# Optimization experiments

Hardware: AMD Instinct MI355X
Metric: run time of the kernel (lower is better)

The kernel has to match this reference:

```python
import jax, jax.numpy as jnp
import numpy as np

RES = 16; NC = 256; NCP = 1024; KNN = 32; SIGMA = 0.1
DM = 256; NH = 8; FF = 1024; NLAYERS = 2
E = NC * 8 * (RES // 8) ** 2
EH = 8
B = 4; N = 65536


def setup_inputs() -> dict:
    key = jax.random.key(0)
    ks = jax.random.split(key, 16)
    s = 0.02
    def w(k, shape):
        return jax.random.normal(k, shape, jnp.float32) * s
    inp = {}
    inp['pc'] = jax.random.normal(ks[0], (B, N, 3), jnp.float32)
    inp['pe_w1'] = w(ks[1], (3, 128)); inp['pe_b1'] = jnp.zeros((128,), jnp.float32)
    inp['pe_w2'] = w(ks[2], (128, 128)); inp['pe_b2'] = jnp.zeros((128,), jnp.float32)
    inp['t_qkv_w'] = w(ks[3], (NLAYERS, DM, 3 * DM)); inp['t_qkv_b'] = jnp.zeros((NLAYERS, 3 * DM), jnp.float32)
    inp['t_out_w'] = w(ks[4], (NLAYERS, DM, DM)); inp['t_out_b'] = jnp.zeros((NLAYERS, DM), jnp.float32)
    inp['t_ln1_s'] = jnp.ones((NLAYERS, DM), jnp.float32); inp['t_ln1_b'] = jnp.zeros((NLAYERS, DM), jnp.float32)
    inp['t_ff1_w'] = w(ks[5], (NLAYERS, DM, FF)); inp['t_ff1_b'] = jnp.zeros((NLAYERS, FF), jnp.float32)
    inp['t_ff2_w'] = w(ks[6], (NLAYERS, FF, DM)); inp['t_ff2_b'] = jnp.zeros((NLAYERS, DM), jnp.float32)
    inp['t_ln2_s'] = jnp.ones((NLAYERS, DM), jnp.float32); inp['t_ln2_b'] = jnp.zeros((NLAYERS, DM), jnp.float32)
    inp['c1_w'] = w(ks[7], (2 * NC, NC, 3, 3)); inp['c1_b'] = jnp.zeros((2 * NC,), jnp.float32)
    inp['c2_w'] = w(ks[8], (4 * NC, 2 * NC, 3, 3)); inp['c2_b'] = jnp.zeros((4 * NC,), jnp.float32)
    inp['c3_w'] = w(ks[9], (8 * NC, 4 * NC, 3, 3)); inp['c3_b'] = jnp.zeros((8 * NC,), jnp.float32)
    inp['x_qkv_w'] = w(ks[10], (E, 3 * E)); inp['x_qkv_b'] = jnp.zeros((3 * E,), jnp.float32)
    inp['x_out_w'] = w(ks[11], (E, E)); inp['x_out_b'] = jnp.zeros((E,), jnp.float32)
    return inp


def _layernorm(x, s, b):
    m = x.mean(-1, keepdims=True)
    v = ((x - m) ** 2).mean(-1, keepdims=True)
    return (x - m) / jnp.sqrt(v + 1e-5) * s + b


def _mha(x, qkv_w, qkv_b, out_w, out_b, nh):
    Bq, S, D = x.shape
    dh = D // nh
    qkv = x @ qkv_w + qkv_b
    q, k, v = jnp.split(qkv, 3, axis=-1)
    def sp(t):
        return t.reshape(Bq, S, nh, dh).transpose(0, 2, 1, 3)
    q, k, v = sp(q), sp(k), sp(v)
    a = jax.nn.softmax(jnp.einsum('bhqd,bhkd->bhqk', q, k) / jnp.sqrt(jnp.float32(dh)), axis=-1)
    o = jnp.einsum('bhqk,bhkd->bhqd', a, v).transpose(0, 2, 1, 3).reshape(Bq, S, D)
    return o @ out_w + out_b


def _density(pc):
    # faithful to source: distance to the FIRST k points (unsorted), not kNN
    d = jnp.linalg.norm(pc[:, :, None, :] - pc[:, None, :KNN, :], axis=-1)  # (B,N,k)
    return jnp.exp(-2.0 * SIGMA ** 2 / (d * d + 1e-6)).mean(axis=-1)


def _fps_indices(pc, density):
    # incremental min-dist FPS: selects identical points to the original O(N*K^2) loop
    def one(pc_b, dens_b):
        first = jnp.argmax(dens_b)
        mind = jnp.linalg.norm(pc_b - pc_b[first], axis=-1)
        def step(mind, _):
            idx = jnp.argmax(mind)
            d = jnp.linalg.norm(pc_b - pc_b[idx], axis=-1)
            return jnp.minimum(mind, d), idx
        _, rest = jax.lax.scan(step, mind, None, length=NCP - 1)
        return jnp.concatenate([first[None], rest])
    return jax.vmap(one)(pc, density)


def _forward(pc, idx, pe_w1, pe_b1, pe_w2, pe_b2, t_qkv_w, t_qkv_b, t_out_w, t_out_b,
             t_ln1_s, t_ln1_b, t_ff1_w, t_ff1_b, t_ff2_w, t_ff2_b, t_ln2_s, t_ln2_b,
             c1_w, c1_b, c2_w, c2_b, c3_w, c3_b, x_qkv_w, x_qkv_b, x_out_w, x_out_b):
    Bq = pc.shape[0]
    centers = jnp.take_along_axis(pc, idx[:, :, None], axis=1)  # (B,K,3)
    # point encoder MLP -> (B,K,128)
    f = jax.nn.relu(centers @ pe_w1 + pe_b1) @ pe_w2 + pe_b2
    # sinusoidal pos-emb per axis, mean over xyz -> (B,K,128)
    half = 64
    freqs = jnp.exp(jnp.arange(half, dtype=jnp.float32) * (-np.log(10000.0) / (half - 1)))
    e = centers[..., None] * freqs  # (B,K,3,64)
    pos = jnp.concatenate([jnp.sin(e), jnp.cos(e)], axis=-1).mean(axis=2)
    x = jnp.concatenate([f, pos], axis=-1)  # (B,K,256)
    # 2-layer post-LN transformer encoder
    for l in range(NLAYERS):
        h = _mha(x, t_qkv_w[l], t_qkv_b[l], t_out_w[l], t_out_b[l], NH)
        x = _layernorm(x + h, t_ln1_s[l], t_ln1_b[l])
        h = jax.nn.relu(x @ t_ff1_w[l] + t_ff1_b[l]) @ t_ff2_w[l] + t_ff2_b[l]
        x = _layernorm(x + h, t_ln2_s[l], t_ln2_b[l])
    # scatter-add features onto three planes
    L = pc.max() - pc.min()
    def grid(c):
        return jnp.clip(((c + L / 2) / L * RES).astype(jnp.int32), 0, RES - 1)
    gx = grid(centers[..., 0]); gy = grid(centers[..., 1]); gz = grid(centers[..., 2])
    tri = jnp.zeros((Bq, 3, RES, RES, DM), jnp.float32)  # channels last for scatter
    bi = jnp.arange(Bq)[:, None]
    tri = tri.at[bi, 0, gy, gx].add(x)
    tri = tri.at[bi, 1, gz, gy].add(x)
    tri = tri.at[bi, 2, gz, gx].add(x)
    tri = tri.transpose(0, 1, 4, 2, 3)  # (B,3,C,R,R)
    z = tri.reshape(Bq * 3, DM, RES, RES)
    def conv(xx, w, b):
        y = jax.lax.conv_general_dilated(xx, w, (2, 2), ((1, 1), (1, 1)),
                                         dimension_numbers=('NCHW', 'OIHW', 'NCHW'))
        return y + b[None, :, None, None]
    z = jax.nn.relu(conv(z, c1_w, c1_b))
    z = jax.nn.relu(conv(z, c2_w, c2_b))
    z = jax.nn.relu(conv(z, c3_w, c3_b))  # (B*3, 8C, R/8, R/8)
    flat = z.reshape(Bq, 3, E)
    attn = _mha(flat, x_qkv_w, x_qkv_b, x_out_w, x_out_b, EH)
    return attn.reshape(Bq, 3, 8 * NC, RES // 8, RES // 8)


def reference(pc, pe_w1, pe_b1, pe_w2, pe_b2, t_qkv_w, t_qkv_b, t_out_w, t_out_b,
              t_ln1_s, t_ln1_b, t_ff1_w, t_ff1_b, t_ff2_w, t_ff2_b, t_ln2_s, t_ln2_b,
              c1_w, c1_b, c2_w, c2_b, c3_w, c3_b, x_qkv_w, x_qkv_b, x_out_w, x_out_b):
    idx = _fps_indices(pc, _density(pc))
    return _forward(pc, idx, pe_w1, pe_b1, pe_w2, pe_b2, t_qkv_w, t_qkv_b, t_out_w, t_out_b,
                    t_ln1_s, t_ln1_b, t_ff1_w, t_ff1_b, t_ff2_w, t_ff2_b, t_ln2_s, t_ln2_b,
                    c1_w, c1_b, c2_w, c2_b, c3_w, c3_b, x_qkv_w, x_qkv_b, x_out_w, x_out_b)
```

## Files before the change

### kernel.cpp

```cpp
#include <hip/hip_runtime.h>
#include <math.h>

#define NPTS   65536
#define NBATCH 4
#define KCP    1024
#define DM     256
#define FFD    1024
#define EDIM   8192
#define N3E    24576

#define FPS_NBLK 16
#define FPS_THR  256
#define FPS_PPT  16
#define GPUB     10
#define HARV_MAX 16
#define RING     16

typedef __attribute__((ext_vector_type(8))) short short8v;
typedef __attribute__((ext_vector_type(4))) short short4v;
typedef __attribute__((ext_vector_type(4))) float float4v;

__device__ __forceinline__ unsigned long long umaxll(unsigned long long a, unsigned long long b) {
  return a > b ? a : b;
}

__device__ __forceinline__ short bf16rn(float f) {
  unsigned u = __float_as_uint(f);
  return (short)((u + 0x7FFFu + ((u >> 16) & 1u)) >> 16);
}

__global__ __launch_bounds__(256) void redmm_kernel(const float* __restrict__ v, int n,
                                                    float* __restrict__ pmax, float* __restrict__ pmin) {
  float mx = -INFINITY, mn = INFINITY;
  for (int i = blockIdx.x * 256 + threadIdx.x; i < n; i += gridDim.x * 256) {
    float x = v[i]; mx = fmaxf(mx, x); mn = fminf(mn, x);
  }
#pragma unroll
  for (int off = 32; off >= 1; off >>= 1) {
    mx = fmaxf(mx, __shfl_xor(mx, off, 64));
    mn = fminf(mn, __shfl_xor(mn, off, 64));
  }
  __shared__ float smx[4], smn[4];
  int lane = threadIdx.x & 63, w = threadIdx.x >> 6;
  if (lane == 0) { smx[w] = mx; smn[w] = mn; }
  __syncthreads();
  if (threadIdx.x == 0) {
    pmax[blockIdx.x] = fmaxf(fmaxf(smx[0], smx[1]), fmaxf(smx[2], smx[3]));
    pmin[blockIdx.x] = fminf(fminf(smn[0], smn[1]), fminf(smn[2], smn[3]));
  }
}

__global__ __launch_bounds__(256) void redfin_kernel(const float* __restrict__ pmax,
                                                     const float* __restrict__ pmin, int nb,
                                                     float* __restrict__ Lv) {
  float mx = -INFINITY, mn = INFINITY;
  for (int i = threadIdx.x; i < nb; i += 256) { mx = fmaxf(mx, pmax[i]); mn = fminf(mn, pmin[i]); }
#pragma unroll
  for (int off = 32; off >= 1; off >>= 1) {
    mx = fmaxf(mx, __shfl_xor(mx, off, 64));
    mn = fminf(mn, __shfl_xor(mn, off, 64));
  }
  __shared__ float smx[4], smn[4];
  int lane = threadIdx.x & 63, w = threadIdx.x >> 6;
  if (lane == 0) { smx[w] = mx; smn[w] = mn; }
  __syncthreads();
  if (threadIdx.x == 0) {
    mx = fmaxf(fmaxf(smx[0], smx[1]), fmaxf(smx[2], smx[3]));
    mn = fminf(fminf(smn[0], smn[1]), fminf(smn[2], smn[3]));
    Lv[0] = __fsub_rn(mx, mn);
  }
}

__global__ __launch_bounds__(FPS_THR, 1) void fps_kernel(const float* __restrict__ pc,
                                                         float* __restrict__ centers,
                                                         unsigned* __restrict__ tags,
                                                         unsigned long long* __restrict__ keys) {
  const int blk = blockIdx.x;
  const int b = blk / FPS_NBLK, bb = blk % FPS_NBLK;
  const int tid = threadIdx.x;
  const int lane = tid & 63, wv = tid >> 6;
  const int wvg = bb * 4 + wv;
  const float* pcb = pc + (size_t)b * NPTS * 3;

  __shared__ float kpts[96];

  float px[FPS_PPT], py[FPS_PPT], pz[FPS_PPT], mind[FPS_PPT];
  const int gbase = wvg * 1024;
#pragma unroll
  for (int i = 0; i < FPS_PPT; ++i) {
    int g = gbase + i * 64 + lane;
    px[i] = pcb[3 * g]; py[i] = pcb[3 * g + 1]; pz[i] = pcb[3 * g + 2];
  }
  for (int i = tid; i < 96; i += FPS_THR) kpts[i] = pcb[i];
  __syncthreads();

  unsigned* const tagb = tags + (size_t)b * RING * 64;
  unsigned long long* const keyb = keys + (size_t)b * RING * 64 * GPUB;

  auto exchange = [&](const unsigned long long* ek, int nk, int r,
                      unsigned long long* ck) {
    const int ri = r & (RING - 1);
    if (lane == 0) {
      unsigned long long* sp = keyb + ((size_t)ri * 64 + wvg) * GPUB;
      for (int g = 0; g < nk; ++g)
        __hip_atomic_store(&sp[g], ek[g], __ATOMIC_RELAXED, __HIP_MEMORY_SCOPE_AGENT);
      __hip_atomic_store(&tagb[ri * 64 + wvg], (unsigned)r, __ATOMIC_RELEASE, __HIP_MEMORY_SCOPE_AGENT);
    }
    unsigned tag;
    do {
      tag = __hip_atomic_load(&tagb[ri * 64 + lane], __ATOMIC_ACQUIRE, __HIP_MEMORY_SCOPE_AGENT);
    } while (__any(tag != (unsigned)r));
    const unsigned long long* pl = keyb + ((size_t)ri * 64 + lane) * GPUB;
    for (int e = 0; e < nk; ++e)
      ck[e] = __hip_atomic_load(&pl[e], __ATOMIC_RELAXED, __HIP_MEMORY_SCOPE_AGENT);
  };

  {
    unsigned long long bk = 0ull;
#pragma unroll
    for (int i = 0; i < FPS_PPT; ++i) {
      float acc = 0.f;
      for (int j = 0; j < 32; ++j) {
        float dx = __fsub_rn(px[i], kpts[3 * j]);
        float dy = __fsub_rn(py[i], kpts[3 * j + 1]);
        float dz = __fsub_rn(pz[i], kpts[3 * j + 2]);
        float ss = __fadd_rn(__fadd_rn(__fmul_rn(dx, dx), __fmul_rn(dy, dy)), __fmul_rn(dz, dz));
        float d = __fsqrt_rn(ss);
        float dd = __fadd_rn(__fmul_rn(d, d), 1e-6f);
        acc = __fadd_rn(acc, expf(__fdiv_rn(-0.02f, dd)));
      }
      float dens = __fdiv_rn(acc, 32.f);
      int g = gbase + i * 64 + lane;
      bk = umaxll(bk, ((unsigned long long)__float_as_uint(dens) << 32) | (unsigned int)(~g));
    }
#pragma unroll
    for (int off = 1; off < 64; off <<= 1) bk = umaxll(bk, __shfl_xor(bk, off, 64));
    unsigned long long ek[1] = { bk }, ck[1];
    exchange(ek, 1, 1, ck);
    unsigned long long k2 = ck[0];
#pragma unroll
    for (int off = 1; off < 64; off <<= 1) k2 = umaxll(k2, __shfl_xor(k2, off, 64));
    int widx = (int)(~(unsigned)(k2 & 0xFFFFFFFFull));
    float wx = pcb[3 * widx], wy = pcb[3 * widx + 1], wz = pcb[3 * widx + 2];
    if (wvg == 0 && lane == 0) {
      centers[(size_t)b * KCP * 3 + 0] = wx;
      centers[(size_t)b * KCP * 3 + 1] = wy;
      centers[(size_t)b * KCP * 3 + 2] = wz;
    }
#pragma unroll
    for (int i = 0; i < FPS_PPT; ++i) {
      float dx = __fsub_rn(px[i], wx), dy = __fsub_rn(py[i], wy), dz = __fsub_rn(pz[i], wz);
      mind[i] = __fsqrt_rn(__fadd_rn(__fadd_rn(__fmul_rn(dx, dx), __fmul_rn(dy, dy)), __fmul_rn(dz, dz)));
    }
  }

  int t = 1;
  for (int r = 2; t < KCP; ++r) {
    unsigned long long tk[FPS_PPT];
#pragma unroll
    for (int i = 0; i < FPS_PPT; ++i) {
      int g = gbase + i * 64 + lane;
      tk[i] = ((unsigned long long)__float_as_uint(mind[i]) << 32) | (unsigned int)(~g);
    }
    unsigned long long ek[GPUB];
#pragma unroll
    for (int g = 0; g < GPUB; ++g) {
      unsigned long long lbk = 0ull;
#pragma unroll
      for (int i = 0; i < FPS_PPT; ++i) lbk = umaxll(lbk, tk[i]);
      unsigned long long wk = lbk;
#pragma unroll
      for (int off = 1; off < 64; off <<= 1) wk = umaxll(wk, __shfl_xor(wk, off, 64));
      ek[g] = wk;
#pragma unroll
      for (int i = 0; i < FPS_PPT; ++i)
        if (tk[i] == wk) tk[i] = 0ull;
    }
    unsigned long long ck[GPUB];
    exchange(ek, GPUB, r, ck);
    float cx[GPUB], cy[GPUB], cz[GPUB];
#pragma unroll
    for (int e = 0; e < GPUB; ++e) {
      int gi = (int)(~(unsigned)(ck[e] & 0xFFFFFFFFull));
      cx[e] = pcb[3 * gi]; cy[e] = pcb[3 * gi + 1]; cz[e] = pcb[3 * gi + 2];
    }
    unsigned long long u = ck[GPUB - 1];
#pragma unroll
    for (int off = 1; off < 64; off <<= 1) u = umaxll(u, __shfl_xor(u, off, 64));
    int h = 0;
    while (true) {
      unsigned long long lb = 0ull; float lx = 0.f, ly = 0.f, lz = 0.f;
#pragma unroll
      for (int e = 0; e < GPUB; ++e)
        if (ck[e] > lb) { lb = ck[e]; lx = cx[e]; ly = cy[e]; lz = cz[e]; }
      unsigned long long wk = lb;
#pragma unroll
      for (int off = 1; off < 64; off <<= 1) wk = umaxll(wk, __shfl_xor(wk, off, 64));
      if (h > 0 && wk < u) break;
      int owner = __ffsll(__ballot(lb == wk)) - 1;
      float wx = __shfl(lx, owner, 64), wy = __shfl(ly, owner, 64), wz = __shfl(lz, owner, 64);
      if (wvg == 0 && lane == 0) {
        centers[((size_t)b * KCP + t) * 3 + 0] = wx;
        centers[((size_t)b * KCP + t) * 3 + 1] = wy;
        centers[((size_t)b * KCP + t) * 3 + 2] = wz;
      }
#pragma unroll
      for (int e = 0; e < GPUB; ++e) {
        float dx = __fsub_rn(cx[e], wx), dy = __fsub_rn(cy[e], wy), dz = __fsub_rn(cz[e], wz);
        float d = __fsqrt_rn(__fadd_rn(__fadd_rn(__fmul_rn(dx, dx), __fmul_rn(dy, dy)), __fmul_rn(dz, dz)));
        float ov = __uint_as_float((unsigned)(ck[e] >> 32));
        float nv = fminf(ov, d);
        ck[e] = ((unsigned long long)__float_as_uint(nv) << 32) | (ck[e] & 0xFFFFFFFFull);
      }
#pragma unroll
      for (int i = 0; i < FPS_PPT; ++i) {
        float dx = __fsub_rn(px[i], wx), dy = __fsub_rn(py[i], wy), dz = __fsub_rn(pz[i], wz);
        float d = __fsqrt_rn(__fadd_rn(__fadd_rn(__fmul_rn(dx, dx), __fmul_rn(dy, dy)), __fmul_rn(dz, dz)));
        mind[i] = fminf(mind[i], d);
      }
      ++h; ++t;
      if (h == HARV_MAX || t == KCP) break;
    }
  }
}

__global__ __launch_bounds__(128) void pe_kernel(const float* __restrict__ centers,
                                                 const float* __restrict__ w1, const float* __restrict__ b1,
                                                 const float* __restrict__ w2, const float* __restrict__ b2,
                                                 float* __restrict__ x) {
  const int p = blockIdx.x;
  const int d = threadIdx.x;
  __shared__ float h[128];
  __shared__ float c[3];
  if (d < 3) c[d] = centers[(size_t)p * 3 + d];
  __syncthreads();
  float hv = b1[d];
#pragma unroll
  for (int j = 0; j < 3; ++j) hv += c[j] * w1[j * 128 + d];
  hv = fmaxf(hv, 0.f);
  h[d] = hv;
  __syncthreads();
  float f = b2[d];
  for (int j = 0; j < 128; ++j) f += h[j] * w2[j * 128 + d];
  x[(size_t)p * 256 + d] = f;
  if (d < 64) {
    float fr = expf(__fmul_rn((float)d, -0.14619587892025696f));
    float ssum = 0.f, csum = 0.f;
#pragma unroll
    for (int a = 0; a < 3; ++a) {
      float e = __fmul_rn(c[a], fr);
      ssum += sinf(e); csum += cosf(e);
    }
    x[(size_t)p * 256 + 128 + d] = __fdiv_rn(ssum, 3.f);
    x[(size_t)p * 256 + 192 + d] = __fdiv_rn(csum, 3.f);
  }
}

__global__ __launch_bounds__(256) void gemm_mfma_kernel(const float* __restrict__ A,
                                                        const float* __restrict__ W,
                                                        const float* __restrict__ bias,
                                                        float* __restrict__ C,
                                                        int M, int Kd, int Nd, int relu) {
  __shared__ short Al[128][40];
  __shared__ short Wl[128][40];
  const int bm = blockIdx.y * 128, bn = blockIdx.x * 128;
  const int tid = threadIdx.x;
  const int lane = tid & 63, wv = tid >> 6;
  const int wr = wv >> 1, wc = wv & 1;
  const int l15 = lane & 15, lk = lane >> 4;

  float4v acc[4][4];
#pragma unroll
  for (int i = 0; i < 4; ++i)
#pragma unroll
    for (int j = 0; j < 4; ++j) acc[i][j] = (float4v){0.f, 0.f, 0.f, 0.f};

  for (int k0 = 0; k0 < Kd; k0 += 32) {
    __syncthreads();
#pragma unroll
    for (int i = 0; i < 4; ++i) {
      int idx = (i * 256 + tid) * 4;
      int m = idx >> 5, k = idx & 31;
      float4 v = *(const float4*)&A[(size_t)(bm + m) * Kd + k0 + k];
      short4v s = { bf16rn(v.x), bf16rn(v.y), bf16rn(v.z), bf16rn(v.w) };
      *(short4v*)&Al[m][k] = s;
    }
#pragma unroll
    for (int i = 0; i < 4; ++i) {
      int task = i * 256 + tid;
      int n = task & 127, c = task >> 7;
      short4v s;
#pragma unroll
      for (int j = 0; j < 4; ++j)
        s[j] = bf16rn(W[(size_t)(k0 + c * 4 + j) * Nd + bn + n]);
      *(short4v*)&Wl[n][c * 4] = s;
    }
    __syncthreads();
    short8v af[4], bf[4];
#pragma unroll
    for (int mf = 0; mf < 4; ++mf)
      af[mf] = *(const short8v*)&Al[wr * 64 + mf * 16 + l15][lk * 8];
#pragma unroll
    for (int nf = 0; nf < 4; ++nf)
      bf[nf] = *(const short8v*)&Wl[wc * 64 + nf * 16 + l15][lk * 8];
#pragma unroll
    for (int mf = 0; mf < 4; ++mf)
#pragma unroll
      for (int nf = 0; nf < 4; ++nf)
        acc[mf][nf] = __builtin_amdgcn_mfma_f32_16x16x32_bf16(af[mf], bf[nf], acc[mf][nf], 0, 0, 0);
  }

#pragma unroll
  for (int mf = 0; mf < 4; ++mf) {
    int row = bm + wr * 64 + mf * 16 + lk * 4;
#pragma unroll
    for (int nf = 0; nf < 4; ++nf) {
      int col = bn + wc * 64 + nf * 16 + l15;
      float bv = bias[col];
#pragma unroll
      for (int j = 0; j < 4; ++j) {
        float v = acc[mf][nf][j] + bv;
        if (relu) v = fmaxf(v, 0.f);
        C[(size_t)(row + j) * Nd + col] = v;
      }
    }
  }
}

__global__ __launch_bounds__(256, 1) void flash_kernel(const float* __restrict__ qkv, float* __restrict__ ao) {
  const int qt = blockIdx.x, h = blockIdx.y, b = blockIdx.z;
  const int tid = threadIdx.x;
  const int qi = tid >> 2, p = tid & 3;
  const int q0 = qt * 64;
  __shared__ float Kc[64][36];
  __shared__ float Vc[64][36];
  __shared__ float Sc[64][68];

  float4 q4[8];
  const float* qrow = qkv + (size_t)(b * 1024 + q0 + qi) * 768 + h * 32;
#pragma unroll
  for (int i = 0; i < 8; ++i) q4[i] = ((const float4*)qrow)[i];

  float o0[4] = {0, 0, 0, 0}, o1[4] = {0, 0, 0, 0};
  float m_cur = -INFINITY, l_part = 0.f;
  const int d0 = p * 8;

  for (int c0 = 0; c0 < 1024; c0 += 64) {
    for (int i = tid; i < 64 * 32; i += 256) {
      int j = i >> 5, d = i & 31;
      size_t row = (size_t)(b * 1024 + c0 + j) * 768;
      Kc[j][d] = qkv[row + 256 + h * 32 + d];
      Vc[j][d] = qkv[row + 512 + h * 32 + d];
    }
    __syncthreads();
    float sreg[16];
#pragma unroll 4
    for (int jj = 0; jj < 16; ++jj) {
      int j = p + 4 * jj;
      const float* kr = &Kc[j][0];
      float s = 0.f;
#pragma unroll
      for (int i = 0; i < 8; ++i) {
        float4 kv = *(const float4*)(kr + 4 * i);
        s += q4[i].x * kv.x + q4[i].y * kv.y + q4[i].z * kv.z + q4[i].w * kv.w;
      }
      sreg[jj] = s * 0.17677669529663687f;
    }
    float cmax = sreg[0];
#pragma unroll
    for (int jj = 1; jj < 16; ++jj) cmax = fmaxf(cmax, sreg[jj]);
    cmax = fmaxf(cmax, __shfl_xor(cmax, 1, 64));
    cmax = fmaxf(cmax, __shfl_xor(cmax, 2, 64));
    float m_new = fmaxf(m_cur, cmax);
    float corr = expf(m_cur - m_new);
    l_part *= corr;
#pragma unroll
    for (int i = 0; i < 4; ++i) { o0[i] *= corr; o1[i] *= corr; }
#pragma unroll
    for (int jj = 0; jj < 16; ++jj) {
      float pv = expf(sreg[jj] - m_new);
      l_part += pv;
      Sc[qi][p + 4 * jj] = pv;
    }
    m_cur = m_new;
    for (int j = 0; j < 64; ++j) {
      float pj = Sc[qi][j];
      float4 va = *(const float4*)(&Vc[j][d0]);
      float4 vb = *(const float4*)(&Vc[j][d0 + 4]);
      o0[0] += pj * va.x; o0[1] += pj * va.y; o0[2] += pj * va.z; o0[3] += pj * va.w;
      o1[0] += pj * vb.x; o1[1] += pj * vb.y; o1[2] += pj * vb.z; o1[3] += pj * vb.w;
    }
    __syncthreads();
  }
  float l2 = l_part + __shfl_xor(l_part, 1, 64);
  float lt = l2 + __shfl_xor(l2, 2, 64);
  float inv = 1.f / lt;
  float* orow = ao + (size_t)(b * 1024 + q0 + qi) * 256 + h * 32 + d0;
#pragma unroll
  for (int i = 0; i < 4; ++i) orow[i] = o0[i] * inv;
#pragma unroll
  for (int i = 0; i < 4; ++i) orow[4 + i] = o1[i] * inv;
}

__global__ __launch_bounds__(256) void ln_kernel(const float* __restrict__ a, const float* __restrict__ r,
                                                 const float* __restrict__ sc, const float* __restrict__ bi,
                                                 float* __restrict__ out) {
  const int row = blockIdx.x * 4 + (threadIdx.x >> 6);
  const int lane = threadIdx.x & 63;
  const float* ar = a + (size_t)row * 256;
  const float* rr = r + (size_t)row * 256;
  float v[4];
#pragma unroll
  for (int i = 0; i < 4; ++i) v[i] = ar[lane + 64 * i] + rr[lane + 64 * i];
  float s = v[0] + v[1] + v[2] + v[3];
#pragma unroll
  for (int off = 32; off >= 1; off >>= 1) s += __shfl_xor(s, off, 64);
  float mean = s * (1.f / 256.f);
  float vs = 0.f;
#pragma unroll
  for (int i = 0; i < 4; ++i) { float d = v[i] - mean; vs += d * d; }
#pragma unroll
  for (int off = 32; off >= 1; off >>= 1) vs += __shfl_xor(vs, off, 64);
  float var = vs * (1.f / 256.f);
  float rstd = 1.f / sqrtf(var + 1e-5f);
  float* orow = out + (size_t)row * 256;
#pragma unroll
  for (int i = 0; i < 4; ++i) {
    int d = lane + 64 * i;
    orow[d] = (v[i] - mean) * rstd * sc[d] + bi[d];
  }
}

__global__ __launch_bounds__(256) void scatter_kernel(const float* __restrict__ x,
                                                      const float* __restrict__ centers,
                                                      const float* __restrict__ Lv,
                                                      float* __restrict__ tri) {
  const int pnt = blockIdx.x;
  const int b = pnt >> 10;
  const int tid = threadIdx.x;
  __shared__ int g[3];
  if (tid == 0) {
    float L = Lv[0];
    float half = __fmul_rn(L, 0.5f);
#pragma unroll
    for (int a = 0; a < 3; ++a) {
      float c = centers[(size_t)pnt * 3 + a];
      float t = __fmul_rn(__fdiv_rn(__fadd_rn(c, half), L), 16.f);
      int gi = (int)t;
      g[a] = min(15, max(0, gi));
    }
  }
  __syncthreads();
  const int gx = g[0], gy = g[1], gz = g[2];
  float v = x[(size_t)pnt * 256 + tid];
  float* trib = tri + (size_t)b * 3 * 256 * 256;
  atomicAdd(&trib[(0 * 256 + tid) * 256 + gy * 16 + gx], v);
  atomicAdd(&trib[(1 * 256 + tid) * 256 + gz * 16 + gy], v);
  atomicAdd(&trib[(2 * 256 + tid) * 256 + gz * 16 + gx], v);
}

template <int IC, int OC, int IH, int IW, int OH, int OW, int OCT, int ICC>
__global__ __launch_bounds__(256, 1) void conv_kernel(const float* __restrict__ in, const float* __restrict__ w,
                                                      const float* __restrict__ bias, float* __restrict__ out) {
  __shared__ float lin[ICC * IH * IW];
  const int n = blockIdx.x;
  const int oc = blockIdx.y * OCT + threadIdx.x / (OH * OW);
  const int sp = threadIdx.x % (OH * OW);
  const int oy = sp / OW, ox = sp % OW;
  const int iy0 = oy * 2 - 1, ix0 = ox * 2 - 1;
  float acc = 0.f;
  for (int c0 = 0; c0 < IC; c0 += ICC) {
    __syncthreads();
    for (int i = threadIdx.x; i < ICC * IH * IW; i += 256)
      lin[i] = in[((size_t)n * IC + c0) * (IH * IW) + i];
    __syncthreads();
    const float* wp = w + ((size_t)oc * IC + c0) * 9;
    for (int ic = 0; ic < ICC; ++ic) {
      const float* wr = wp + (size_t)ic * 9;
      const float* lr = lin + ic * IH * IW;
#pragma unroll
      for (int ky = 0; ky < 3; ++ky) {
        int iy = iy0 + ky;
        if (iy >= 0 && iy < IH) {
#pragma unroll
          for (int kx = 0; kx < 3; ++kx) {
            int ix = ix0 + kx;
            if (ix >= 0 && ix < IW) acc += lr[iy * IW + ix] * wr[ky * 3 + kx];
          }
        }
      }
    }
  }
  out[((size_t)n * OC + oc) * (OH * OW) + sp] = fmaxf(acc + bias[oc], 0.f);
}

__global__ void biasinit_kernel(float* __restrict__ out, const float* __restrict__ bias, int M, int N) {
  int i = blockIdx.x * 256 + threadIdx.x;
  if (i < M * N) out[i] = bias[i % N];
}

template <int M, int KC>
__global__ __launch_bounds__(256, 1) void matvec_kernel(const float* __restrict__ A, const float* __restrict__ W,
                                                        float* __restrict__ out, int Kd, int Nd) {
  __shared__ float Al[KC * M];
  const int tid = threadIdx.x;
  const int n = blockIdx.x * 256 + tid;
  const int k0 = blockIdx.y * KC;
  for (int i = tid; i < KC * M; i += 256) {
    int k = i / M, m = i - k * M;
    Al[i] = A[(size_t)m * Kd + k0 + k];
  }
  __syncthreads();
  float acc[M] = {};
  for (int k = 0; k < KC; ++k) {
    float wv = W[(size_t)(k0 + k) * Nd + n];
#pragma unroll
    for (int m = 0; m < M; ++m) acc[m] += Al[k * M + m] * wv;
  }
#pragma unroll
  for (int m = 0; m < M; ++m) atomicAdd(&out[(size_t)m * Nd + n], acc[m]);
}

__global__ __launch_bounds__(256) void attn3_kernel(const float* __restrict__ qkv, float* __restrict__ o) {
  const int b = blockIdx.x >> 3, h = blockIdx.x & 7;
  const float* base = qkv + (size_t)b * 3 * N3E;
  const int qo = h * 1024, ko = EDIM + h * 1024, vo = 2 * EDIM + h * 1024;
  float p[9] = {};
  for (int d = threadIdx.x; d < 1024; d += 256) {
    float q0 = base[qo + d], q1 = base[N3E + qo + d], q2 = base[2 * N3E + qo + d];
    float k0 = base[ko + d], k1 = base[N3E + ko + d], k2 = base[2 * N3E + ko + d];
    p[0] += q0 * k0; p[1] += q0 * k1; p[2] += q0 * k2;
    p[3] += q1 * k0; p[4] += q1 * k1; p[5] += q1 * k2;
    p[6] += q2 * k0; p[7] += q2 * k1; p[8] += q2 * k2;
  }
  __shared__ float red[4][9];
  __shared__ float aw[9];
  const int lane = threadIdx.x & 63, w = threadIdx.x >> 6;
#pragma unroll
  for (int e = 0; e < 9; ++e)
#pragma unroll
    for (int off = 32; off >= 1; off >>= 1) p[e] += __shfl_xor(p[e], off, 64);
  if (lane == 0)
#pragma unroll
    for (int e = 0; e < 9; ++e) red[w][e] = p[e];
  __syncthreads();
  if (threadIdx.x == 0) {
    float s[9];
#pragma unroll
    for (int e = 0; e < 9; ++e) s[e] = (red[0][e] + red[1][e] + red[2][e] + red[3][e]) / 32.f;
#pragma unroll
    for (int i = 0; i < 3; ++i) {
      float m = fmaxf(fmaxf(s[i * 3], s[i * 3 + 1]), s[i * 3 + 2]);
      float e0 = expf(s[i * 3] - m), e1 = expf(s[i * 3 + 1] - m), e2 = expf(s[i * 3 + 2] - m);
      float sm = e0 + e1 + e2;
      aw[i * 3] = e0 / sm; aw[i * 3 + 1] = e1 / sm; aw[i * 3 + 2] = e2 / sm;
    }
  }
  __syncthreads();
  for (int d = threadIdx.x; d < 1024; d += 256) {
    float v0 = base[vo + d], v1 = base[N3E + vo + d], v2 = base[2 * N3E + vo + d];
#pragma unroll
    for (int i = 0; i < 3; ++i)
      o[(size_t)(b * 3 + i) * EDIM + h * 1024 + d] = aw[i * 3] * v0 + aw[i * 3 + 1] * v1 + aw[i * 3 + 2] * v2;
  }
}

extern "C" void kernel_launch(void* const* d_in, const int* in_sizes, int n_in,
                              void* d_out, int out_size, void* d_ws, size_t ws_size,
                              hipStream_t stream) {
  const float* pc      = (const float*)d_in[0];
  const float* pe_w1   = (const float*)d_in[1];
  const float* pe_b1   = (const float*)d_in[2];
  const float* pe_w2   = (const float*)d_in[3];
  const float* pe_b2   = (const float*)d_in[4];
  const float* t_qkv_w = (const float*)d_in[5];
  const float* t_qkv_b = (const float*)d_in[6];
  const float* t_out_w = (const float*)d_in[7];
  const float* t_out_b = (const float*)d_in[8];
  const float* t_ln1_s = (const float*)d_in[9];
  const float* t_ln1_b = (const float*)d_in[10];
  const float* t_ff1_w = (const float*)d_in[11];
  const float* t_ff1_b = (const float*)d_in[12];
  const float* t_ff2_w = (const float*)d_in[13];
  const float* t_ff2_b = (const float*)d_in[14];
  const float* t_ln2_s = (const float*)d_in[15];
  const float* t_ln2_b = (const float*)d_in[16];
  const float* c1_w    = (const float*)d_in[17];
  const float* c1_b    = (const float*)d_in[18];
  const float* c2_w    = (const float*)d_in[19];
  const float* c2_b    = (const float*)d_in[20];
  const float* c3_w    = (const float*)d_in[21];
  const float* c3_b    = (const float*)d_in[22];
  const float* x_qkv_w = (const float*)d_in[23];
  const float* x_qkv_b = (const float*)d_in[24];
  const float* x_out_w = (const float*)d_in[25];
  const float* x_out_b = (const float*)d_in[26];
  float* outp = (float*)d_out;

  char* wsp = (char*)d_ws;
  auto alloc = [&](size_t bytes) { char* q = wsp; wsp += (bytes + 255) & ~(size_t)255; return q; };
  float* centers = (float*)alloc((size_t)NBATCH * KCP * 3 * 4);
  float* pmax    = (float*)alloc(512 * 4);
  float* pmin    = (float*)alloc(512 * 4);
  float* Lv      = (float*)alloc(256);
  unsigned* tags = (unsigned*)alloc((size_t)NBATCH * RING * 64 * 4);
  unsigned long long* keyss = (unsigned long long*)alloc((size_t)NBATCH * RING * 64 * GPUB * 8);
  float* x  = (float*)alloc((size_t)4096 * 256 * 4);
  float* xb = (float*)alloc((size_t)4096 * 256 * 4);
  float* arena = (float*)wsp;
  float* qkvb = arena;
  float* ao   = qkvb + (size_t)4096 * 768;
  float* po   = ao + (size_t)4096 * 256;
  float* ffh  = po + (size_t)4096 * 256;
  float* ffo  = ffh + (size_t)4096 * 1024;
  float* tri  = arena;
  float* z1   = tri + (size_t)NBATCH * 3 * 256 * 256;
  float* z2   = z1 + (size_t)12 * 512 * 64;
  float* z3   = z2 + (size_t)12 * 1024 * 16;
  float* qkv2 = z3 + (size_t)12 * 8192;
  float* at2  = qkv2 + (size_t)12 * N3E;
  (void)in_sizes; (void)n_in; (void)out_size; (void)ws_size; (void)ffo;

  hipMemsetAsync(tags, 0, (size_t)NBATCH * RING * 64 * 4, stream);
  hipMemsetAsync(keyss, 0, (size_t)NBATCH * RING * 64 * GPUB * 8, stream);

  redmm_kernel<<<512, 256, 0, stream>>>(pc, NBATCH * NPTS * 3, pmax, pmin);
  redfin_kernel<<<1, 256, 0, stream>>>(pmax, pmin, 512, Lv);

  fps_kernel<<<NBATCH * FPS_NBLK, FPS_THR, 0, stream>>>(pc, centers, tags, keyss);

  pe_kernel<<<NBATCH * KCP, 128, 0, stream>>>(centers, pe_w1, pe_b1, pe_w2, pe_b2, x);

  for (int l = 0; l < 2; ++l) {
    gemm_mfma_kernel<<<dim3(6, 32), 256, 0, stream>>>(x, t_qkv_w + (size_t)l * 256 * 768,
                                                      t_qkv_b + (size_t)l * 768, qkvb, 4096, 256, 768, 0);
    flash_kernel<<<dim3(16, 8, 4), 256, 0, stream>>>(qkvb, ao);
    gemm_mfma_kernel<<<dim3(2, 32), 256, 0, stream>>>(ao, t_out_w + (size_t)l * 256 * 256,
                                                      t_out_b + (size_t)l * 256, po, 4096, 256, 256, 0);
    ln_kernel<<<1024, 256, 0, stream>>>(x, po, t_ln1_s + (size_t)l * 256, t_ln1_b + (size_t)l * 256, xb);
    gemm_mfma_kernel<<<dim3(8, 32), 256, 0, stream>>>(xb, t_ff1_w + (size_t)l * 256 * 1024,
                                                      t_ff1_b + (size_t)l * 1024, ffh, 4096, 256, 1024, 1);
    gemm_mfma_kernel<<<dim3(2, 32), 256, 0, stream>>>(ffh, t_ff2_w + (size_t)l * 1024 * 256,
                                                      t_ff2_b + (size_t)l * 256, ffo, 4096, 1024, 256, 0);
    ln_kernel<<<1024, 256, 0, stream>>>(xb, ffo, t_ln2_s + (size_t)l * 256, t_ln2_b + (size_t)l * 256, x);
  }

  hipMemsetAsync(tri, 0, (size_t)NBATCH * 3 * 256 * 256 * 4, stream);
  scatter_kernel<<<NBATCH * KCP, 256, 0, stream>>>(x, centers, Lv, tri);

  conv_kernel<256, 512, 16, 16, 8, 8, 4, 32><<<dim3(12, 128), 256, 0, stream>>>(tri, c1_w, c1_b, z1);
  conv_kernel<512, 1024, 8, 8, 4, 4, 16, 128><<<dim3(12, 64), 256, 0, stream>>>(z1, c2_w, c2_b, z2);
  conv_kernel<1024, 2048, 4, 4, 2, 2, 64, 256><<<dim3(12, 32), 256, 0, stream>>>(z2, c3_w, c3_b, z3);

  biasinit_kernel<<<(12 * N3E + 255) / 256, 256, 0, stream>>>(qkv2, x_qkv_b, 12, N3E);
  matvec_kernel<12, 512><<<dim3(N3E / 256, 16), 256, 0, stream>>>(z3, x_qkv_w, qkv2, EDIM, N3E);

  attn3_kernel<<<32, 256, 0, stream>>>(qkv2, at2);

  biasinit_kernel<<<(12 * EDIM + 255) / 256, 256, 0, stream>>>(outp, x_out_b, 12, EDIM);
  matvec_kernel<12, 512><<<dim3(EDIM / 256, 16), 256, 0, stream>>>(at2, x_out_w, outp, EDIM, EDIM);
}
```

Measured before the change: 5.219 ms.

## Rewrite transformer flash attention with bf16 MFMA and tune FPS GPUB

Replaces the scalar-FMA flash attention kernel with one that converts Q, K and V to bf16 in LDS and computes both QK^T and PV with 16x16x32 bf16 MFMA instructions. Online softmax is now done per MFMA row fragment using cross-lane shuffles. The aim is to move the attention math onto the matrix cores, at the cost of bf16 rounding of Q, K, V and P. It also lowers the FPS GPUB constant from 10 to 8 and adds 16-byte alignment to the GEMM LDS tiles.

After: 4.824 ms. 7.6% less time.

```diff
diff --git a/kernel.cpp b/kernel.cpp
--- a/kernel.cpp
+++ b/kernel.cpp
@@ -12,7 +12,7 @@
 #define FPS_NBLK 16
 #define FPS_THR  256
 #define FPS_PPT  16
-#define GPUB     10
+#define GPUB     8
 #define HARV_MAX 16
 #define RING     16
 
@@ -261,8 +261,8 @@
                                                         const float* __restrict__ bias,
                                                         float* __restrict__ C,
                                                         int M, int Kd, int Nd, int relu) {
-  __shared__ short Al[128][40];
-  __shared__ short Wl[128][40];
+  __shared__ __align__(16) short Al[128][40];
+  __shared__ __align__(16) short Wl[128][40];
   const int bm = blockIdx.y * 128, bn = blockIdx.x * 128;
   const int tid = threadIdx.x;
   const int lane = tid & 63, wv = tid >> 6;
@@ -327,79 +327,112 @@
   }
 }
 
-__global__ __launch_bounds__(256, 1) void flash_kernel(const float* __restrict__ qkv, float* __restrict__ ao) {
+__global__ __launch_bounds__(256, 1) void flash_mfma_kernel(const float* __restrict__ qkv,
+                                                            float* __restrict__ ao) {
   const int qt = blockIdx.x, h = blockIdx.y, b = blockIdx.z;
   const int tid = threadIdx.x;
-  const int qi = tid >> 2, p = tid & 3;
+  const int lane = tid & 63, w = tid >> 6;
+  const int l15 = lane & 15, lk = lane >> 4;
   const int q0 = qt * 64;
-  __shared__ float Kc[64][36];
-  __shared__ float Vc[64][36];
-  __shared__ float Sc[64][68];
-
-  float4 q4[8];
-  const float* qrow = qkv + (size_t)(b * 1024 + q0 + qi) * 768 + h * 32;
-#pragma unroll
-  for (int i = 0; i < 8; ++i) q4[i] = ((const float4*)qrow)[i];
-
-  float o0[4] = {0, 0, 0, 0}, o1[4] = {0, 0, 0, 0};
-  float m_cur = -INFINITY, l_part = 0.f;
-  const int d0 = p * 8;
+
+  __shared__ __align__(16) short Kc[64][40];
+  __shared__ __align__(16) short Vt[32][72];
+  __shared__ __align__(16) short Plds[4][16][72];
+
+  short8v qa;
+  {
+    const float* qr = qkv + (size_t)(b * 1024 + q0 + w * 16 + l15) * 768 + h * 32 + lk * 8;
+    float4 a = *(const float4*)qr;
+    float4 c = *(const float4*)(qr + 4);
+    qa = (short8v){ bf16rn(a.x), bf16rn(a.y), bf16rn(a.z), bf16rn(a.w),
+                    bf16rn(c.x), bf16rn(c.y), bf16rn(c.z), bf16rn(c.w) };
+  }
+
+  float4v o0 = (float4v){0.f, 0.f, 0.f, 0.f};
+  float4v o1 = (float4v){0.f, 0.f, 0.f, 0.f};
+  float m_cur[4] = { -INFINITY, -INFINITY, -INFINITY, -INFINITY };
+  float l_part[4] = { 0.f, 0.f, 0.f, 0.f };
+  const float scale = 0.17677669529663687f;
 
   for (int c0 = 0; c0 < 1024; c0 += 64) {
-    for (int i = tid; i < 64 * 32; i += 256) {
-      int j = i >> 5, d = i & 31;
-      size_t row = (size_t)(b * 1024 + c0 + j) * 768;
-      Kc[j][d] = qkv[row + 256 + h * 32 + d];
-      Vc[j][d] = qkv[row + 512 + h * 32 + d];
-    }
     __syncthreads();
-    float sreg[16];
-#pragma unroll 4
-    for (int jj = 0; jj < 16; ++jj) {
-      int j = p + 4 * jj;
-      const float* kr = &Kc[j][0];
-      float s = 0.f;
-#pragma unroll
-      for (int i = 0; i < 8; ++i) {
-        float4 kv = *(const float4*)(kr + 4 * i);
-        s += q4[i].x * kv.x + q4[i].y * kv.y + q4[i].z * kv.z + q4[i].w * kv.w;
+    {
+      int key = tid >> 2, dblk = (tid & 3) * 8;
+      size_t row = (size_t)(b * 1024 + c0 + key) * 768 + h * 32 + dblk;
+      float4 k1 = *(const float4*)&qkv[row + 256];
+      float4 k2 = *(const float4*)&qkv[row + 260];
+      short8v ks = (short8v){ bf16rn(k1.x), bf16rn(k1.y), bf16rn(k1.z), bf16rn(k1.w),
+                              bf16rn(k2.x), bf16rn(k2.y), bf16rn(k2.z), bf16rn(k2.w) };
+      *(short8v*)&Kc[key][dblk] = ks;
+      float4 v1 = *(const float4*)&qkv[row + 512];
+      float4 v2 = *(const float4*)&qkv[row + 516];
+      Vt[dblk + 0][key] = bf16rn(v1.x); Vt[dblk + 1][key] = bf16rn(v1.y);
+      Vt[dblk + 2][key] = bf16rn(v1.z); Vt[dblk + 3][key] = bf16rn(v1.w);
+      Vt[dblk + 4][key] = bf16rn(v2.x); Vt[dblk + 5][key] = bf16rn(v2.y);
+      Vt[dblk + 6][key] = bf16rn(v2.z); Vt[dblk + 7][key] = bf16rn(v2.w);
+    }
+    __syncthreads();
+
+    float4v s[4];
+#pragma unroll
+    for (int f = 0; f < 4; ++f) {
+      short8v kb = *(const short8v*)&Kc[f * 16 + l15][lk * 8];
+      float4v z = (float4v){0.f, 0.f, 0.f, 0.f};
+      s[f] = __builtin_amdgcn_mfma_f32_16x16x32_bf16(qa, kb, z, 0, 0, 0);
+    }
+#pragma unroll
+    for (int f = 0; f < 4; ++f)
+#pragma unroll
+      for (int j = 0; j < 4; ++j) s[f][j] *= scale;
+
+    float corr[4];
+#pragma unroll
+    for (int j = 0; j < 4; ++j) {
+      float v = fmaxf(fmaxf(s[0][j], s[1][j]), fmaxf(s[2][j], s[3][j]));
+#pragma unroll
+      for (int off = 1; off < 16; off <<= 1) v = fmaxf(v, __shfl_xor(v, off, 64));
+      float m_new = fmaxf(m_cur[j], v);
+      corr[j] = expf(m_cur[j] - m_new);
+      m_cur[j] = m_new;
+    }
+#pragma unroll
+    for (int f = 0; f < 4; ++f)
+#pragma unroll
+      for (int j = 0; j < 4; ++j) {
+        float p = expf(s[f][j] - m_cur[j]);
+        s[f][j] = p;
+        Plds[w][lk * 4 + j][f * 16 + l15] = bf16rn(p);
       }
-      sreg[jj] = s * 0.17677669529663687f;
-    }
-    float cmax = sreg[0];
-#pragma unroll
-    for (int jj = 1; jj < 16; ++jj) cmax = fmaxf(cmax, sreg[jj]);
-    cmax = fmaxf(cmax, __shfl_xor(cmax, 1, 64));
-    cmax = fmaxf(cmax, __shfl_xor(cmax, 2, 64));
-    float m_new = fmaxf(m_cur, cmax);
-    float corr = expf(m_cur - m_new);
-    l_part *= corr;
-#pragma unroll
-    for (int i = 0; i < 4; ++i) { o0[i] *= corr; o1[i] *= corr; }
-#pragma unroll
-    for (int jj = 0; jj < 16; ++jj) {
-      float pv = expf(sreg[jj] - m_new);
-      l_part += pv;
-      Sc[qi][p + 4 * jj] = pv;
-    }
-    m_cur = m_new;
-    for (int j = 0; j < 64; ++j) {
-      float pj = Sc[qi][j];
-      float4 va = *(const float4*)(&Vc[j][d0]);
-      float4 vb = *(const float4*)(&Vc[j][d0 + 4]);
-      o0[0] += pj * va.x; o0[1] += pj * va.y; o0[2] += pj * va.z; o0[3] += pj * va.w;
-      o1[0] += pj * vb.x; o1[1] += pj * vb.y; o1[2] += pj * vb.z; o1[3] += pj * vb.w;
-    }
-    __syncthreads();
-  }
-  float l2 = l_part + __shfl_xor(l_part, 1, 64);
-  float lt = l2 + __shfl_xor(l2, 2, 64);
-  float inv = 1.f / lt;
-  float* orow = ao + (size_t)(b * 1024 + q0 + qi) * 256 + h * 32 + d0;
-#pragma unroll
-  for (int i = 0; i < 4; ++i) orow[i] = o0[i] * inv;
-#pragma unroll
-  for (int i = 0; i < 4; ++i) orow[4 + i] = o1[i] * inv;
+#pragma unroll
+    for (int j = 0; j < 4; ++j) {
+      float tsum = s[0][j] + s[1][j] + s[2][j] + s[3][j];
+#pragma unroll
+      for (int off = 1; off < 16; off <<= 1) tsum += __shfl_xor(tsum, off, 64);
+      l_part[j] = l_part[j] * corr[j] + tsum;
+      o0[j] *= corr[j];
+      o1[j] *= corr[j];
+    }
+    asm volatile("s_waitcnt lgkmcnt(0)" ::: "memory");
+    __builtin_amdgcn_sched_barrier(0);
+
+#pragma unroll
+    for (int kb = 0; kb < 2; ++kb) {
+      short8v pa = *(const short8v*)&Plds[w][l15][kb * 32 + lk * 8];
+      short8v vb0 = *(const short8v*)&Vt[l15][kb * 32 + lk * 8];
+      short8v vb1 = *(const short8v*)&Vt[16 + l15][kb * 32 + lk * 8];
+      o0 = __builtin_amdgcn_mfma_f32_16x16x32_bf16(pa, vb0, o0, 0, 0, 0);
+      o1 = __builtin_amdgcn_mfma_f32_16x16x32_bf16(pa, vb1, o1, 0, 0, 0);
+    }
+  }
+
+#pragma unroll
+  for (int j = 0; j < 4; ++j) {
+    float inv = 1.f / l_part[j];
+    int q = q0 + w * 16 + lk * 4 + j;
+    float* orow = ao + (size_t)(b * 1024 + q) * 256 + h * 32;
+    orow[l15] = o0[j] * inv;
+    orow[16 + l15] = o1[j] * inv;
+  }
 }
 
 __global__ __launch_bounds__(256) void ln_kernel(const float* __restrict__ a, const float* __restrict__ r,
@@ -634,7 +667,7 @@
   for (int l = 0; l < 2; ++l) {
     gemm_mfma_kernel<<<dim3(6, 32), 256, 0, stream>>>(x, t_qkv_w + (size_t)l * 256 * 768,
                                                       t_qkv_b + (size_t)l * 768, qkvb, 4096, 256, 768, 0);
-    flash_kernel<<<dim3(16, 8, 4), 256, 0, stream>>>(qkvb, ao);
+    flash_mfma_kernel<<<dim3(16, 8, 4), 256, 0, stream>>>(qkvb, ao);
     gemm_mfma_kernel<<<dim3(2, 32), 256, 0, stream>>>(ao, t_out_w + (size_t)l * 256 * 256,
                                                       t_out_b + (size_t)l * 256, po, 4096, 256, 256, 0);
     ln_kernel<<<1024, 256, 0, stream>>>(x, po, t_ln1_s + (size_t)l * 256, t_ln1_b + (size_t)l * 256, xb);
```
